# Performance work log

Measured on AMD Instinct MI355X. Metric: run time of the kernel, lower is better.

## Reference

```python
import jax, jax.numpy as jnp
import numpy as np

D_MODEL = 1024
D_STATE = 64
D_CONV = 4
HEADDIM = 64
EXPAND = 2
NGROUPS = 1
D_INNER = EXPAND * D_MODEL            # 2048
NHEADS = D_INNER // HEADDIM           # 32
CONV_DIM = D_INNER + 2 * NGROUPS * D_STATE
D_IN_PROJ = 2 * D_INNER + 2 * NGROUPS * D_STATE + NHEADS
FFN_DIM = 4096
B_SZ = 2
SEQ = 2048


def layernorm(x, w, b, eps=1e-5):
    m = jnp.mean(x, axis=-1, keepdims=True)
    v = jnp.var(x, axis=-1, keepdims=True)
    return (x - m) * jax.lax.rsqrt(v + eps) * w + b


def silu(x):
    return x * jax.nn.sigmoid(x)


def causal_dwconv(x, w, b):
    # x: [B, L, C], w: [C, K] depthwise, b: [C]; causal (left) padding
    xc = jnp.transpose(x, (0, 2, 1))                       # [B, C, L]
    xc = jnp.pad(xc, ((0, 0), (0, 0), (D_CONV - 1, 0)))
    k = w[:, None, :]                                      # [C, 1, K]
    y = jax.lax.conv_general_dilated(
        xc, k, window_strides=(1,), padding='VALID',
        dimension_numbers=('NCH', 'OIH', 'NCH'),
        feature_group_count=CONV_DIM)
    return jnp.transpose(y, (0, 2, 1)) + b                 # [B, L, C]


def mamba2(x, in_proj_w, conv_w, conv_b, dt_bias, A_log, D_param, norm_w, out_proj_w):
    Bsz, L, _ = x.shape
    zxbcdt = x @ in_proj_w.T                               # [B, L, D_IN_PROJ]
    z, xBC, dt = jnp.split(zxbcdt, [D_INNER, D_INNER + CONV_DIM], axis=-1)
    dt = jax.nn.softplus(dt + dt_bias)                     # [B, L, H]
    xBC = silu(causal_dwconv(xBC, conv_w, conv_b))
    xs, Bm, Cm = jnp.split(xBC, [D_INNER, D_INNER + NGROUPS * D_STATE], axis=-1)
    xs = xs.reshape(Bsz, L, NHEADS, HEADDIM)
    Bm = Bm.reshape(Bsz, L, NGROUPS, D_STATE)
    Cm = Cm.reshape(Bsz, L, NGROUPS, D_STATE)
    hpg = NHEADS // NGROUPS
    Bh = jnp.repeat(Bm, hpg, axis=2)                       # [B, L, H, N]
    Ch = jnp.repeat(Cm, hpg, axis=2)                       # [B, L, H, N]
    A = -jnp.exp(A_log)                                    # [H]
    dA = jnp.exp(dt * A)                                   # [B, L, H]

    # time-major for scan
    def step(h, inp):
        dA_t, dt_t, x_t, B_t, C_t = inp                    # [B,H], [B,H], [B,H,P], [B,H,N], [B,H,N]
        h = h * dA_t[:, :, None, None] + (dt_t[:, :, None, None] * x_t[..., None]) * B_t[:, :, None, :]
        y_t = jnp.einsum('bhpn,bhn->bhp', h, C_t)
        return h, y_t

    h0 = jnp.zeros((Bsz, NHEADS, HEADDIM, D_STATE), dtype=x.dtype)
    xs_tm = (jnp.moveaxis(dA, 1, 0), jnp.moveaxis(dt, 1, 0),
             jnp.moveaxis(xs, 1, 0), jnp.moveaxis(Bh, 1, 0), jnp.moveaxis(Ch, 1, 0))
    _, ys = jax.lax.scan(step, h0, xs_tm)                  # [L, B, H, P]
    y = jnp.moveaxis(ys, 0, 1) + D_param[None, None, :, None] * xs
    y = y.reshape(Bsz, L, D_INNER)
    # gated RMSNorm: RMSNorm(y * silu(z)) * weight
    y = y * silu(z)
    y = y * jax.lax.rsqrt(jnp.mean(jnp.square(y), axis=-1, keepdims=True) + 1e-5) * norm_w
    return y @ out_proj_w.T                                # [B, L, D_MODEL]


def setup_inputs() -> dict:
    key = jax.random.key(0)
    ks = jax.random.split(key, 12)
    s = 0.02
    inp = {
        'x': jax.random.normal(ks[0], (B_SZ, SEQ, D_MODEL), dtype=jnp.float32),
        'ln0_w': jnp.ones((D_MODEL,), jnp.float32), 'ln0_b': jnp.zeros((D_MODEL,), jnp.float32),
        'ln1_w': jnp.ones((D_MODEL,), jnp.float32), 'ln1_b': jnp.zeros((D_MODEL,), jnp.float32),
        'ln2_w': jnp.ones((D_MODEL,), jnp.float32), 'ln2_b': jnp.zeros((D_MODEL,), jnp.float32),
        'in_proj_w': jax.random.normal(ks[1], (D_IN_PROJ, D_MODEL), jnp.float32) * s,
        'conv_w': jax.random.normal(ks[2], (CONV_DIM, D_CONV), jnp.float32) * 0.2,
        'conv_b': jnp.zeros((CONV_DIM,), jnp.float32),
        'dt_bias': jax.random.uniform(ks[3], (NHEADS,), jnp.float32, -4.0, -1.0),
        'A_log': jnp.log(jnp.arange(1, NHEADS + 1, dtype=jnp.float32)),
        'D_param': jnp.ones((NHEADS,), jnp.float32),
        'norm_w': jnp.ones((D_INNER,), jnp.float32),
        'out_proj_w': jax.random.normal(ks[4], (D_MODEL, D_INNER), jnp.float32) * s,
        'ffn_w1': jax.random.normal(ks[5], (FFN_DIM, D_MODEL), jnp.float32) * s,
        'ffn_b1': jnp.zeros((FFN_DIM,), jnp.float32),
        'ffn_w2': jax.random.normal(ks[6], (D_MODEL, FFN_DIM), jnp.float32) * s,
        'ffn_b2': jnp.zeros((D_MODEL,), jnp.float32),
    }
    return inp


def reference(x, ln0_w, ln0_b, ln1_w, ln1_b, ln2_w, ln2_b, in_proj_w, conv_w, conv_b,
              dt_bias, A_log, D_param, norm_w, out_proj_w, ffn_w1, ffn_b1, ffn_w2, ffn_b2):
    x = layernorm(x, ln0_w, ln0_b)                                  # ln0 (layer_id==0)
    m = mamba2(layernorm(x, ln1_w, ln1_b), in_proj_w, conv_w, conv_b,
               dt_bias, A_log, D_param, norm_w, out_proj_w)
    x = x + m                                                        # dropout is identity in eval
    h = layernorm(x, ln2_w, ln2_b)
    h = jax.nn.gelu(h @ ffn_w1.T + ffn_b1, approximate=False) @ ffn_w2.T + ffn_b2
    return x + h
```

## Files before the change

### kernel.cpp

```cpp
#include <hip/hip_runtime.h>
#include <hip/hip_bf16.h>
#include <math.h>

typedef __hip_bfloat16 bf16;
typedef __bf16 bhalf;
typedef bhalf bhalf8 __attribute__((ext_vector_type(8)));
typedef float f32x4 __attribute__((ext_vector_type(4)));
typedef unsigned short u16;
typedef u16 u16x4 __attribute__((ext_vector_type(4)));

#define D_MODEL   1024
#define D_STATE   64
#define HEADDIM   64
#define D_INNER   2048
#define NHEADS    32
#define CONV_DIM  2176
#define D_IN_PROJ 4256
#define FFN_DIM   4096
#define BSZ       2
#define SEQ       2048
#define NROWS     (BSZ*SEQ)
#define TC        64
#define NCH       (SEQ/TC)

#define AS1 __attribute__((address_space(1)))
#define AS3 __attribute__((address_space(3)))
__device__ __forceinline__ void load_lds16(const void* g, void* l) {
  __builtin_amdgcn_global_load_lds((AS1 void*)g, (AS3 void*)l, 16, 0, 0);
}

__global__ __launch_bounds__(64)
void detect_kernel(const unsigned short* __restrict__ x, int* __restrict__ flagp)
{
  int bad = 0;
  for (int i = threadIdx.x; i < 4096; i += 64) {
    unsigned u = ((unsigned)x[i]) << 16;
    float v = __uint_as_float(u);
    if (!(fabsf(v) <= 1e6f)) bad = 1;
  }
  unsigned long long any = __ballot(bad);
  if (threadIdx.x == 0) *flagp = (any != 0ULL) ? 1 : 0;
}

#define NT 19
struct CvtArgs {
  const void* src[NT];
  void*       dst[NT];
  int ccum[NT + 1];
  int nel[NT];
};

__global__ __launch_bounds__(256)
void cvt_kernel(CvtArgs a, const int* __restrict__ flagp)
{
  int c = blockIdx.x;
  int ti = 0;
  while (c >= a.ccum[ti + 1]) ti++;
  int base = (c - a.ccum[ti]) * 2048;
  int n = a.nel[ti];
  if (*flagp) {
    const float* s = (const float*)a.src[ti];
    bf16* d = (bf16*)a.dst[ti];
    for (int i = threadIdx.x; i < 2048; i += 256) {
      int j = base + i;
      if (j < n) d[j] = __float2bfloat16(s[j]);
    }
  } else {
    const unsigned short* s = (const unsigned short*)a.src[ti];
    unsigned short* d = (unsigned short*)a.dst[ti];
    for (int i = threadIdx.x; i < 2048; i += 256) {
      int j = base + i;
      if (j < n) d[j] = s[j];
    }
  }
}

template<int EPI>
__global__ __launch_bounds__(256, 2)
void gemm_bt(const bf16* __restrict__ A, const bf16* __restrict__ W,
             int M, int N, int K, int nb,
             bf16* __restrict__ outB,
             const bf16* __restrict__ bias)
{
  __shared__ __align__(16) bhalf sA[128 * 64];
  __shared__ __align__(16) bhalf sW[128 * 64];
  const int id   = blockIdx.x;
  const int per  = nb * 8;
  const int hi   = id / per;
  const int rem  = id - hi * per;
  const int jn   = rem >> 3;
  const int mi   = hi * 8 + (rem & 7);
  const int n0   = jn * 128;
  const int m0   = mi * 128;
  const int t    = threadIdx.x;
  const int w    = t >> 6;
  const int lane = t & 63;
  const int wm   = (w >> 1) * 64;
  const int wn   = (w & 1) * 64;
  const int lr   = lane & 15;
  const int lq   = lane >> 4;

  f32x4 acc[4][4];
  #pragma unroll
  for (int i = 0; i < 4; i++)
    #pragma unroll
    for (int j = 0; j < 4; j++)
      acc[i][j] = (f32x4){0.f, 0.f, 0.f, 0.f};

  for (int k0 = 0; k0 < K; k0 += 64) {
    #pragma unroll
    for (int j = 0; j < 4; j++) {
      int s  = t + 256 * j;
      int r  = s >> 3;
      int cs = (s & 7) ^ (r & 7);
      load_lds16(A + (size_t)(m0 + r) * K + k0 + cs * 8, sA + s * 8);
      int wr = n0 + r; wr = wr < N ? wr : N - 1;
      load_lds16(W + (size_t)wr * K + k0 + cs * 8, sW + s * 8);
    }
    __syncthreads();
    #pragma unroll
    for (int kk = 0; kk < 2; kk++) {
      bhalf8 af[4], bfr[4];
      #pragma unroll
      for (int i = 0; i < 4; i++) {
        int r = wm + i * 16 + lr;
        int c = (kk * 4 + lq) ^ (r & 7);
        af[i] = *(const bhalf8*)(sA + r * 64 + c * 8);
      }
      #pragma unroll
      for (int j = 0; j < 4; j++) {
        int r = wn + j * 16 + lr;
        int c = (kk * 4 + lq) ^ (r & 7);
        bfr[j] = *(const bhalf8*)(sW + r * 64 + c * 8);
      }
      #pragma unroll
      for (int i = 0; i < 4; i++)
        #pragma unroll
        for (int j = 0; j < 4; j++)
          acc[i][j] = __builtin_amdgcn_mfma_f32_16x16x32_bf16(af[i], bfr[j], acc[i][j], 0, 0, 0);
    }
    __syncthreads();
  }

  #pragma unroll
  for (int i = 0; i < 4; i++) {
    #pragma unroll
    for (int j = 0; j < 4; j++) {
      #pragma unroll
      for (int r = 0; r < 4; r++) {
        int m = m0 + wm + i * 16 + lq * 4 + r;
        int n = n0 + wn + j * 16 + lr;
        if (n < N) {
          float v = acc[i][j][r];
          size_t idx = (size_t)m * N + n;
          if (EPI == 0) {
            outB[idx] = __float2bfloat16(v);
          } else {
            v += __bfloat162float(bias[n]);
            outB[idx] = __float2bfloat16(0.5f * v * (1.0f + erff(v * 0.70710678118654752f)));
          }
        }
      }
    }
  }
}

template<int EPI>
__global__ __launch_bounds__(256, 2)
void gemm_skinny(const bf16* __restrict__ A, const bf16* __restrict__ W,
                 int M, int N, int K,
                 float* __restrict__ outF, void* __restrict__ outAny,
                 const bf16* __restrict__ bias,
                 const bf16* __restrict__ resB,
                 const float* __restrict__ resF,
                 const int* __restrict__ flagp)
{
  __shared__ __align__(16) bhalf sA[64 * 64];
  __shared__ __align__(16) bhalf sW[128 * 64];
  const int id   = blockIdx.x;
  const int hi   = id >> 6;
  const int rem  = id & 63;
  const int jn   = rem >> 3;
  const int mi   = hi * 8 + (rem & 7);
  const int m0   = mi * 64;
  const int n0   = jn * 128;
  const int t    = threadIdx.x;
  const int w    = t >> 6;
  const int lane = t & 63;
  const int wm   = (w >> 1) * 32;
  const int wn   = (w & 1) * 64;
  const int lr   = lane & 15;
  const int lq   = lane >> 4;

  f32x4 acc[2][4];
  #pragma unroll
  for (int i = 0; i < 2; i++)
    #pragma unroll
    for (int j = 0; j < 4; j++)
      acc[i][j] = (f32x4){0.f, 0.f, 0.f, 0.f};

  for (int k0 = 0; k0 < K; k0 += 64) {
    {
      #pragma unroll
      for (int j = 0; j < 2; j++) {
        int s  = t + 256 * j;
        int r  = s >> 3;
        int cs = (s & 7) ^ (r & 7);
        load_lds16(A + (size_t)(m0 + r) * K + k0 + cs * 8, sA + s * 8);
      }
      #pragma unroll
      for (int j = 0; j < 4; j++) {
        int s  = t + 256 * j;
        int r  = s >> 3;
        int cs = (s & 7) ^ (r & 7);
        load_lds16(W + (size_t)(n0 + r) * K + k0 + cs * 8, sW + s * 8);
      }
    }
    __syncthreads();
    #pragma unroll
    for (int kk = 0; kk < 2; kk++) {
      bhalf8 af[2], bfr[4];
      #pragma unroll
      for (int i = 0; i < 2; i++) {
        int r = wm + i * 16 + lr;
        int c = (kk * 4 + lq) ^ (r & 7);
        af[i] = *(const bhalf8*)(sA + r * 64 + c * 8);
      }
      #pragma unroll
      for (int j = 0; j < 4; j++) {
        int r = wn + j * 16 + lr;
        int c = (kk * 4 + lq) ^ (r & 7);
        bfr[j] = *(const bhalf8*)(sW + r * 64 + c * 8);
      }
      #pragma unroll
      for (int i = 0; i < 2; i++)
        #pragma unroll
        for (int j = 0; j < 4; j++)
          acc[i][j] = __builtin_amdgcn_mfma_f32_16x16x32_bf16(af[i], bfr[j], acc[i][j], 0, 0, 0);
    }
    __syncthreads();
  }

  const bool f32o = (EPI == 1) && (*flagp != 0);
  #pragma unroll
  for (int i = 0; i < 2; i++) {
    #pragma unroll
    for (int j = 0; j < 4; j++) {
      #pragma unroll
      for (int r = 0; r < 4; r++) {
        int m = m0 + wm + i * 16 + lq * 4 + r;
        int n = n0 + wn + j * 16 + lr;
        size_t idx = (size_t)m * N + n;
        float v = acc[i][j][r];
        if (EPI == 0) {
          outF[idx] = v + __bfloat162float(resB[idx]);
        } else {
          v += __bfloat162float(bias[n]) + resF[idx];
          if (f32o) ((float*)outAny)[idx] = v;
          else      ((bf16*)outAny)[idx] = __float2bfloat16(v);
        }
      }
    }
  }
}

__global__ __launch_bounds__(256)
void ln01_kernel(const bf16* __restrict__ x,
                 const bf16* __restrict__ w0, const bf16* __restrict__ b0,
                 const bf16* __restrict__ w1, const bf16* __restrict__ b1,
                 bf16* __restrict__ x0o, bf16* __restrict__ x1o)
{
  int row = blockIdx.x, t = threadIdx.x;
  const bf16* xr = x + (size_t)row * D_MODEL;
  __shared__ float rs[4], rq[4];
  float v[4], s = 0.f, ss = 0.f;
  #pragma unroll
  for (int i = 0; i < 4; i++) {
    v[i] = __bfloat162float(xr[t + 256 * i]);
    s += v[i]; ss += v[i] * v[i];
  }
  #pragma unroll
  for (int o = 32; o; o >>= 1) { s += __shfl_down(s, o); ss += __shfl_down(ss, o); }
  if ((t & 63) == 0) { rs[t >> 6] = s; rq[t >> 6] = ss; }
  __syncthreads();
  float S = rs[0] + rs[1] + rs[2] + rs[3];
  float Q = rq[0] + rq[1] + rq[2] + rq[3];
  float mean = S * (1.f / D_MODEL);
  float rstd = rsqrtf(Q * (1.f / D_MODEL) - mean * mean + 1e-5f);
  float u[4]; s = 0.f; ss = 0.f;
  #pragma unroll
  for (int i = 0; i < 4; i++) {
    int c = t + 256 * i;
    u[i] = (v[i] - mean) * rstd * __bfloat162float(w0[c]) + __bfloat162float(b0[c]);
    s += u[i]; ss += u[i] * u[i];
    x0o[(size_t)row * D_MODEL + c] = __float2bfloat16(u[i]);
  }
  __syncthreads();
  #pragma unroll
  for (int o = 32; o; o >>= 1) { s += __shfl_down(s, o); ss += __shfl_down(ss, o); }
  if ((t & 63) == 0) { rs[t >> 6] = s; rq[t >> 6] = ss; }
  __syncthreads();
  S = rs[0] + rs[1] + rs[2] + rs[3];
  Q = rq[0] + rq[1] + rq[2] + rq[3];
  mean = S * (1.f / D_MODEL);
  rstd = rsqrtf(Q * (1.f / D_MODEL) - mean * mean + 1e-5f);
  #pragma unroll
  for (int i = 0; i < 4; i++) {
    int c = t + 256 * i;
    x1o[(size_t)row * D_MODEL + c] =
        __float2bfloat16((u[i] - mean) * rstd * __bfloat162float(w1[c]) + __bfloat162float(b1[c]));
  }
}

__global__ __launch_bounds__(256)
void conv_silu_kernel(const bf16* __restrict__ zxb, const bf16* __restrict__ cw,
                      const bf16* __restrict__ cb, bf16* __restrict__ xact)
{
  int c = blockIdx.x * 256 + threadIdx.x;
  int row = blockIdx.y;
  if (c >= CONV_DIM) return;
  int l = row & (SEQ - 1);
  float acc = __bfloat162float(cb[c]);
  #pragma unroll
  for (int k = 0; k < 4; k++) {
    int lt = l - 3 + k;
    if (lt >= 0)
      acc += __bfloat162float(zxb[(size_t)(row - 3 + k) * D_IN_PROJ + D_INNER + c]) *
             __bfloat162float(cw[c * 4 + k]);
  }
  xact[(size_t)row * CONV_DIM + c] = __float2bfloat16(acc / (1.f + expf(-acc)));
}

__global__ __launch_bounds__(256)
void dt_kernel(const bf16* __restrict__ zxb, const bf16* __restrict__ dt_bias,
               const bf16* __restrict__ A_log, float* __restrict__ dts,
               float* __restrict__ ldab)
{
  int i = blockIdx.x * 256 + threadIdx.x;
  int row = i >> 5, h = i & 31;
  float v = __bfloat162float(zxb[(size_t)row * D_IN_PROJ + (D_INNER + CONV_DIM) + h]) +
            __bfloat162float(dt_bias[h]);
  float sp = (v > 20.f) ? v : log1pf(expf(v));
  dts[i] = sp;
  ldab[i] = -sp * expf(__bfloat162float(A_log[h]));
}

__global__ __launch_bounds__(256)
void scan_state_kernel(const bf16* __restrict__ xact, const float* __restrict__ dts,
                       const float* __restrict__ ldab, bf16* __restrict__ Sbuf,
                       float* __restrict__ acb)
{
  __shared__ __align__(16) bf16 wBT[64][72];
  __shared__ __align__(16) bf16 XT[64][72];
  __shared__ float lsS[64], dtS[64];
  const int bid = blockIdx.x;
  const int bh = bid & 63, c = bid >> 6;
  const int b = bh >> 5, h = bh & 31;
  const int t0 = c * TC;
  const int tid = threadIdx.x;
  const int w = tid >> 6, lane = tid & 63;
  const int lr = lane & 15, lq = lane >> 4;

  if (w == 0) {
    float v = ldab[(size_t)(b * SEQ + t0 + lane) * NHEADS + h];
    #pragma unroll
    for (int o = 1; o < 64; o <<= 1) {
      float up = __shfl_up(v, o);
      if (lane >= o) v += up;
    }
    lsS[lane] = v;
    dtS[lane] = dts[(size_t)(b * SEQ + t0 + lane) * NHEADS + h];
  }
  __syncthreads();
  const float lsT = lsS[63];
  {
    int nn = tid & 63, u0 = (tid >> 6) * 16;
    for (int i = 0; i < 16; i++) {
      int u = u0 + i;
      const bf16* rowp = xact + (size_t)(b * SEQ + t0 + u) * CONV_DIM;
      float wgt = dtS[u] * __expf(lsT - lsS[u]);
      wBT[nn][u] = __float2bfloat16(__bfloat162float(rowp[D_INNER + nn]) * wgt);
      XT[nn][u]  = rowp[h * 64 + nn];
    }
  }
  __syncthreads();

  bhalf8 af0 = *(const bhalf8*)&wBT[16 * w + lr][lq * 8];
  bhalf8 af1 = *(const bhalf8*)&wBT[16 * w + lr][32 + lq * 8];
  bf16* sb = Sbuf + ((size_t)bh * NCH + c) * 4096;
  #pragma unroll
  for (int jt = 0; jt < 4; jt++) {
    bhalf8 xf0 = *(const bhalf8*)&XT[16 * jt + lr][lq * 8];
    bhalf8 xf1 = *(const bhalf8*)&XT[16 * jt + lr][32 + lq * 8];
    f32x4 acc = (f32x4){0.f, 0.f, 0.f, 0.f};
    acc = __builtin_amdgcn_mfma_f32_16x16x32_bf16(af0, xf0, acc, 0, 0, 0);
    acc = __builtin_amdgcn_mfma_f32_16x16x32_bf16(af1, xf1, acc, 0, 0, 0);
    #pragma unroll
    for (int r = 0; r < 4; r++) {
      int n = 16 * w + lq * 4 + r;
      int p = 16 * jt + lr;
      sb[p * 64 + n] = __float2bfloat16(acc[r]);
    }
  }
  if (tid == 0) acb[bh * NCH + c] = __expf(lsT);
}

__global__ __launch_bounds__(256)
void state_prop_kernel(bf16* __restrict__ Sbuf, const float* __restrict__ acb)
{
  const int bh = blockIdx.x >> 2, q = blockIdx.x & 3;
  const int t = threadIdx.x;
  bf16* sp = Sbuf + (size_t)bh * NCH * 4096 + q * 1024 + t;
  const float* ap = acb + bh * NCH;
  float h0 = 0.f, h1 = 0.f, h2 = 0.f, h3 = 0.f;
  for (int c = 0; c < NCH; c++) {
    bf16* pc = sp + (size_t)c * 4096;
    float s0 = __bfloat162float(pc[0]);
    float s1 = __bfloat162float(pc[256]);
    float s2 = __bfloat162float(pc[512]);
    float s3 = __bfloat162float(pc[768]);
    float a = ap[c];
    pc[0]   = __float2bfloat16(h0);
    pc[256] = __float2bfloat16(h1);
    pc[512] = __float2bfloat16(h2);
    pc[768] = __float2bfloat16(h3);
    h0 = fmaf(h0, a, s0); h1 = fmaf(h1, a, s1);
    h2 = fmaf(h2, a, s2); h3 = fmaf(h3, a, s3);
  }
}

__global__ __launch_bounds__(256)
void scan_y_kernel(const bf16* __restrict__ xact, const float* __restrict__ dts,
                   const float* __restrict__ ldab, const bf16* __restrict__ Sbuf,
                   bf16* __restrict__ yfull)
{
  __shared__ __align__(16) bf16 Cs[64][72];
  __shared__ __align__(16) bf16 Bs[64][72];
  __shared__ __align__(16) bf16 XT[64][72];
  __shared__ __align__(16) bf16 HT[64][72];
  __shared__ __align__(16) bf16 Ms[64][72];
  __shared__ float lsS[64], dtS[64];
  const int bid = blockIdx.x;
  const int bh = bid & 63, c = bid >> 6;
  const int b = bh >> 5, h = bh & 31;
  const int t0 = c * TC;
  const int tid = threadIdx.x;
  const int w = tid >> 6, lane = tid & 63;
  const int lr = lane & 15, lq = lane >> 4;

  if (w == 0) {
    float v = ldab[(size_t)(b * SEQ + t0 + lane) * NHEADS + h];
    #pragma unroll
    for (int o = 1; o < 64; o <<= 1) {
      float up = __shfl_up(v, o);
      if (lane >= o) v += up;
    }
    lsS[lane] = v;
    dtS[lane] = dts[(size_t)(b * SEQ + t0 + lane) * NHEADS + h];
  }
  {
    int nn = tid & 63, u0 = (tid >> 6) * 16;
    for (int i = 0; i < 16; i++) {
      int u = u0 + i;
      const bf16* rowp = xact + (size_t)(b * SEQ + t0 + u) * CONV_DIM;
      Bs[u][nn] = rowp[D_INNER + nn];
      Cs[u][nn] = rowp[D_INNER + 64 + nn];
      XT[nn][u] = rowp[h * 64 + nn];
    }
    const bf16* sb = Sbuf + ((size_t)bh * NCH + c) * 4096;
    for (int i = 0; i < 16; i++) {
      int e = tid + 256 * i;
      HT[e >> 6][e & 63] = sb[e];
    }
  }
  __syncthreads();

  bhalf8 cf0 = *(const bhalf8*)&Cs[16 * w + lr][lq * 8];
  bhalf8 cf1 = *(const bhalf8*)&Cs[16 * w + lr][32 + lq * 8];
  f32x4 accH[4];
  #pragma unroll
  for (int jt = 0; jt < 4; jt++) {
    bhalf8 bf0 = *(const bhalf8*)&Bs[16 * jt + lr][lq * 8];
    bhalf8 bf1 = *(const bhalf8*)&Bs[16 * jt + lr][32 + lq * 8];
    f32x4 g = (f32x4){0.f, 0.f, 0.f, 0.f};
    g = __builtin_amdgcn_mfma_f32_16x16x32_bf16(cf0, bf0, g, 0, 0, 0);
    g = __builtin_amdgcn_mfma_f32_16x16x32_bf16(cf1, bf1, g, 0, 0, 0);
    bhalf8 hf0 = *(const bhalf8*)&HT[16 * jt + lr][lq * 8];
    bhalf8 hf1 = *(const bhalf8*)&HT[16 * jt + lr][32 + lq * 8];
    f32x4 ah = (f32x4){0.f, 0.f, 0.f, 0.f};
    ah = __builtin_amdgcn_mfma_f32_16x16x32_bf16(cf0, hf0, ah, 0, 0, 0);
    ah = __builtin_amdgcn_mfma_f32_16x16x32_bf16(cf1, hf1, ah, 0, 0, 0);
    accH[jt] = ah;
    #pragma unroll
    for (int r = 0; r < 4; r++) {
      int t = 16 * w + lq * 4 + r;
      int u = 16 * jt + lr;
      float m = 0.f;
      if (u <= t) m = g[r] * __expf(lsS[t] - lsS[u]) * dtS[u];
      Ms[t][u] = __float2bfloat16(m);
    }
  }
  __syncthreads();

  bhalf8 mf0 = *(const bhalf8*)&Ms[16 * w + lr][lq * 8];
  bhalf8 mf1 = *(const bhalf8*)&Ms[16 * w + lr][32 + lq * 8];
  #pragma unroll
  for (int jt = 0; jt < 4; jt++) {
    bhalf8 xf0 = *(const bhalf8*)&XT[16 * jt + lr][lq * 8];
    bhalf8 xf1 = *(const bhalf8*)&XT[16 * jt + lr][32 + lq * 8];
    f32x4 acc = (f32x4){0.f, 0.f, 0.f, 0.f};
    acc = __builtin_amdgcn_mfma_f32_16x16x32_bf16(mf0, xf0, acc, 0, 0, 0);
    acc = __builtin_amdgcn_mfma_f32_16x16x32_bf16(mf1, xf1, acc, 0, 0, 0);
    #pragma unroll
    for (int r = 0; r < 4; r++) {
      int t = 16 * w + lq * 4 + r;
      int p = 16 * jt + lr;
      float y = acc[r] + __expf(lsS[t]) * accH[jt][r];
      yfull[(size_t)(b * SEQ + t0 + t) * D_INNER + h * 64 + p] = __float2bfloat16(y);
    }
  }
}

__global__ __launch_bounds__(256)
void gate_rms_kernel(const bf16* __restrict__ yfull, const bf16* __restrict__ xact,
                     const bf16* __restrict__ zxb, const bf16* __restrict__ Dp,
                     const bf16* __restrict__ nw, bf16* __restrict__ yn)
{
  int row = blockIdx.x, t = threadIdx.x;
  __shared__ float rq[4];
  float yv[8]; float ss = 0.f;
  #pragma unroll
  for (int i = 0; i < 8; i++) {
    int c = t + 256 * i;
    float y = __bfloat162float(yfull[(size_t)row * D_INNER + c]) +
              __bfloat162float(Dp[c >> 6]) *
              __bfloat162float(xact[(size_t)row * CONV_DIM + c]);
    float z = __bfloat162float(zxb[(size_t)row * D_IN_PROJ + c]);
    yv[i] = y * (z / (1.f + expf(-z)));
    ss += yv[i] * yv[i];
  }
  #pragma unroll
  for (int o = 32; o; o >>= 1) ss += __shfl_down(ss, o);
  if ((t & 63) == 0) rq[t >> 6] = ss;
  __syncthreads();
  float tot = rq[0] + rq[1] + rq[2] + rq[3];
  float rr = rsqrtf(tot * (1.f / D_INNER) + 1e-5f);
  #pragma unroll
  for (int i = 0; i < 8; i++) {
    int c = t + 256 * i;
    yn[(size_t)row * D_INNER + c] =
        __float2bfloat16(yv[i] * rr * __bfloat162float(nw[c]));
  }
}

__global__ __launch_bounds__(256)
void ln2_kernel(const float* __restrict__ xin, const bf16* __restrict__ w,
                const bf16* __restrict__ b, bf16* __restrict__ out)
{
  int row = blockIdx.x, t = threadIdx.x;
  const float* xr = xin + (size_t)row * D_MODEL;
  __shared__ float rs[4], rq[4];
  float v[4], s = 0.f, ss = 0.f;
  #pragma unroll
  for (int i = 0; i < 4; i++) {
    v[i] = xr[t + 256 * i];
    s += v[i]; ss += v[i] * v[i];
  }
  #pragma unroll
  for (int o = 32; o; o >>= 1) { s += __shfl_down(s, o); ss += __shfl_down(ss, o); }
  if ((t & 63) == 0) { rs[t >> 6] = s; rq[t >> 6] = ss; }
  __syncthreads();
  float S = rs[0] + rs[1] + rs[2] + rs[3];
  float Q = rq[0] + rq[1] + rq[2] + rq[3];
  float mean = S * (1.f / D_MODEL);
  float rstd = rsqrtf(Q * (1.f / D_MODEL) - mean * mean + 1e-5f);
  #pragma unroll
  for (int i = 0; i < 4; i++) {
    int c = t + 256 * i;
    out[(size_t)row * D_MODEL + c] =
        __float2bfloat16((v[i] - mean) * rstd * __bfloat162float(w[c]) + __bfloat162float(b[c]));
  }
}

extern "C" void kernel_launch(void* const* d_in, const int* in_sizes, int n_in,
                              void* d_out, int out_size, void* d_ws, size_t ws_size,
                              hipStream_t stream)
{
  char* ws = (char*)d_ws;
  bf16*  xcvt  = (bf16*) (ws + 0);
  bf16*  x1b   = (bf16*) (ws + 8388608);
  bf16*  Sbuf  = (bf16*) (ws + 0);
  bf16*  ynb   = (bf16*) (ws + 0);
  bf16*  wproj = (bf16*) (ws + 16777216);
  float* acb   = (float*)(ws + 16777216);
  float* dtsb  = (float*)(ws + 16785408);
  float* ldab  = (float*)(ws + 17309696);
  bf16*  wout  = (bf16*) (ws + 25493504);
  bf16*  w1c   = (bf16*) (ws + 29687808);
  bf16*  w2c   = (bf16*) (ws + 38076416);
  bf16*  ln0w  = (bf16*) (ws + 46465024);
  bf16*  ln0b  = (bf16*) (ws + 46467072);
  bf16*  ln1w  = (bf16*) (ws + 46469120);
  bf16*  ln1b  = (bf16*) (ws + 46471168);
  bf16*  ln2w  = (bf16*) (ws + 46473216);
  bf16*  ln2b  = (bf16*) (ws + 46475264);
  bf16*  convw = (bf16*) (ws + 46477312);
  bf16*  convb = (bf16*) (ws + 46494720);
  bf16*  dtb   = (bf16*) (ws + 46499072);
  bf16*  alog  = (bf16*) (ws + 46499136);
  bf16*  Dp    = (bf16*) (ws + 46499200);
  bf16*  normw = (bf16*) (ws + 46499264);
  bf16*  b1c   = (bf16*) (ws + 46503360);
  bf16*  b2c   = (bf16*) (ws + 46511552);
  int*   flag  = (int*)  (ws + 46513600);
  bf16*  x0b   = (bf16*) (ws + 46514176);
  bf16*  zxb   = (bf16*) (ws + 54902784);
  float* x2f   = (float*)(ws + 54902784);
  bf16*  xact  = (bf16*) (ws + 89767936);
  bf16*  gbuf  = (bf16*) (ws + 89767936);
  bf16*  yfull = (bf16*) (ws + 125419520);
  bf16*  hln   = (bf16*) (ws + 125419520);

  detect_kernel<<<1, 64, 0, stream>>>((const unsigned short*)d_in[0], flag);

  CvtArgs ca;
  void* dsts[NT] = { xcvt, ln0w, ln0b, ln1w, ln1b, ln2w, ln2b, wproj, convw, convb,
                     dtb, alog, Dp, normw, wout, w1c, b1c, w2c, b2c };
  int cc = 0;
  ca.ccum[0] = 0;
  for (int i = 0; i < NT; i++) {
    ca.src[i] = d_in[i];
    ca.dst[i] = dsts[i];
    ca.nel[i] = in_sizes[i];
    cc += (in_sizes[i] + 2047) / 2048;
    ca.ccum[i + 1] = cc;
  }
  cvt_kernel<<<cc, 256, 0, stream>>>(ca, flag);

  ln01_kernel<<<NROWS, 256, 0, stream>>>(xcvt, ln0w, ln0b, ln1w, ln1b, x0b, x1b);

  gemm_bt<0><<<34 * 32, 256, 0, stream>>>(x1b, wproj, NROWS, D_IN_PROJ, D_MODEL, 34,
                                          zxb, nullptr);

  conv_silu_kernel<<<dim3(9, NROWS), 256, 0, stream>>>(zxb, convw, convb, xact);
  dt_kernel<<<(NROWS * NHEADS) / 256, 256, 0, stream>>>(zxb, dtb, alog, dtsb, ldab);

  scan_state_kernel<<<NCH * 64, 256, 0, stream>>>(xact, dtsb, ldab, Sbuf, acb);
  state_prop_kernel<<<64 * 4, 256, 0, stream>>>(Sbuf, acb);
  scan_y_kernel<<<NCH * 64, 256, 0, stream>>>(xact, dtsb, ldab, Sbuf, yfull);

  gate_rms_kernel<<<NROWS, 256, 0, stream>>>(yfull, xact, zxb, Dp, normw, ynb);

  gemm_skinny<0><<<512, 256, 0, stream>>>(ynb, wout, NROWS, D_MODEL, D_INNER,
                                          x2f, nullptr, nullptr, x0b, nullptr, flag);

  ln2_kernel<<<NROWS, 256, 0, stream>>>(x2f, ln2w, ln2b, hln);

  gemm_bt<2><<<32 * 32, 256, 0, stream>>>(hln, w1c, NROWS, FFN_DIM, D_MODEL, 32,
                                          gbuf, b1c);

  gemm_skinny<1><<<512, 256, 0, stream>>>(gbuf, w2c, NROWS, D_MODEL, FFN_DIM,
                                          nullptr, d_out, b2c, nullptr, x2f, flag);
}
```

Measured before the change: 477.8 us.

## Split-K skinny GEMMs with fused reduce+LN2, fuse conv/dt, skip x conversion

The two N=1024 GEMMs now split K in half and launch 1024 blocks, with occupancy hint 4, to fill more CUs. Each half writes fp32 partials, and separate reduce kernels add them together with the residual and bias. The out-proj reduce also performs LayerNorm2. The dt computation is folded into the conv+SiLU kernel, and ln01 reads the raw input directly instead of a converted copy. The split adds fp32 partial traffic and extra launches in exchange for better GEMM parallelism.

```diff
diff --git a/kernel.cpp b/kernel.cpp
--- a/kernel.cpp
+++ b/kernel.cpp
@@ -42,7 +42,7 @@
   if (threadIdx.x == 0) *flagp = (any != 0ULL) ? 1 : 0;
 }
 
-#define NT 19
+#define NT 18
 struct CvtArgs {
   const void* src[NT];
   void*       dst[NT];
@@ -165,21 +165,18 @@
   }
 }
 
-template<int EPI>
-__global__ __launch_bounds__(256, 2)
-void gemm_skinny(const bf16* __restrict__ A, const bf16* __restrict__ W,
-                 int M, int N, int K,
-                 float* __restrict__ outF, void* __restrict__ outAny,
-                 const bf16* __restrict__ bias,
-                 const bf16* __restrict__ resB,
-                 const float* __restrict__ resF,
-                 const int* __restrict__ flagp)
+__global__ __launch_bounds__(256, 4)
+void gemm_skinny_sk(const bf16* __restrict__ A, const bf16* __restrict__ W,
+                    int M, int N, int K,
+                    float* __restrict__ p0, float* __restrict__ p1)
 {
   __shared__ __align__(16) bhalf sA[64 * 64];
   __shared__ __align__(16) bhalf sW[128 * 64];
   const int id   = blockIdx.x;
-  const int hi   = id >> 6;
-  const int rem  = id & 63;
+  const int z    = id >> 9;
+  const int id9  = id & 511;
+  const int hi   = id9 >> 6;
+  const int rem  = id9 & 63;
   const int jn   = rem >> 3;
   const int mi   = hi * 8 + (rem & 7);
   const int m0   = mi * 64;
@@ -199,22 +196,22 @@
     for (int j = 0; j < 4; j++)
       acc[i][j] = (f32x4){0.f, 0.f, 0.f, 0.f};
 
-  for (int k0 = 0; k0 < K; k0 += 64) {
-    {
-      #pragma unroll
-      for (int j = 0; j < 2; j++) {
-        int s  = t + 256 * j;
-        int r  = s >> 3;
-        int cs = (s & 7) ^ (r & 7);
-        load_lds16(A + (size_t)(m0 + r) * K + k0 + cs * 8, sA + s * 8);
-      }
-      #pragma unroll
-      for (int j = 0; j < 4; j++) {
-        int s  = t + 256 * j;
-        int r  = s >> 3;
-        int cs = (s & 7) ^ (r & 7);
-        load_lds16(W + (size_t)(n0 + r) * K + k0 + cs * 8, sW + s * 8);
-      }
+  const int kh = K >> 1;
+  const int kend = z * kh + kh;
+  for (int k0 = z * kh; k0 < kend; k0 += 64) {
+    #pragma unroll
+    for (int j = 0; j < 2; j++) {
+      int s  = t + 256 * j;
+      int r  = s >> 3;
+      int cs = (s & 7) ^ (r & 7);
+      load_lds16(A + (size_t)(m0 + r) * K + k0 + cs * 8, sA + s * 8);
+    }
+    #pragma unroll
+    for (int j = 0; j < 4; j++) {
+      int s  = t + 256 * j;
+      int r  = s >> 3;
+      int cs = (s & 7) ^ (r & 7);
+      load_lds16(W + (size_t)(n0 + r) * K + k0 + cs * 8, sW + s * 8);
     }
     __syncthreads();
     #pragma unroll
@@ -241,44 +238,102 @@
     __syncthreads();
   }
 
-  const bool f32o = (EPI == 1) && (*flagp != 0);
-  #pragma unroll
-  for (int i = 0; i < 2; i++) {
-    #pragma unroll
-    for (int j = 0; j < 4; j++) {
+  float* out = z ? p1 : p0;
+  #pragma unroll
+  for (int i = 0; i < 2; i++)
+    #pragma unroll
+    for (int j = 0; j < 4; j++)
       #pragma unroll
       for (int r = 0; r < 4; r++) {
         int m = m0 + wm + i * 16 + lq * 4 + r;
         int n = n0 + wn + j * 16 + lr;
-        size_t idx = (size_t)m * N + n;
-        float v = acc[i][j][r];
-        if (EPI == 0) {
-          outF[idx] = v + __bfloat162float(resB[idx]);
-        } else {
-          v += __bfloat162float(bias[n]) + resF[idx];
-          if (f32o) ((float*)outAny)[idx] = v;
-          else      ((bf16*)outAny)[idx] = __float2bfloat16(v);
-        }
+        out[(size_t)m * N + n] = acc[i][j][r];
       }
-    }
-  }
-}
-
-__global__ __launch_bounds__(256)
-void ln01_kernel(const bf16* __restrict__ x,
+}
+
+__global__ __launch_bounds__(256)
+void reduce_out_ln2_kernel(const float* __restrict__ p0, const float* __restrict__ p1,
+                           const bf16* __restrict__ resB, float* __restrict__ x2f,
+                           const bf16* __restrict__ w, const bf16* __restrict__ b,
+                           bf16* __restrict__ hln)
+{
+  int row = blockIdx.x, t = threadIdx.x;
+  int i = row * 256 + t;
+  __shared__ float rs[4], rq[4];
+  f32x4 a = ((const f32x4*)p0)[i];
+  f32x4 bb = ((const f32x4*)p1)[i];
+  u16x4 r = ((const u16x4*)resB)[i];
+  f32x4 o;
+  float s = 0.f, ss = 0.f;
+  #pragma unroll
+  for (int j = 0; j < 4; j++) {
+    o[j] = a[j] + bb[j] + __uint_as_float(((unsigned)r[j]) << 16);
+    s += o[j]; ss += o[j] * o[j];
+  }
+  ((f32x4*)x2f)[i] = o;
+  #pragma unroll
+  for (int off = 32; off; off >>= 1) { s += __shfl_down(s, off); ss += __shfl_down(ss, off); }
+  if ((t & 63) == 0) { rs[t >> 6] = s; rq[t >> 6] = ss; }
+  __syncthreads();
+  float S = rs[0] + rs[1] + rs[2] + rs[3];
+  float Q = rq[0] + rq[1] + rq[2] + rq[3];
+  float mean = S * (1.f / D_MODEL);
+  float rstd = rsqrtf(Q * (1.f / D_MODEL) - mean * mean + 1e-5f);
+  u16x4 wv = ((const u16x4*)w)[t];
+  u16x4 bv = ((const u16x4*)b)[t];
+  #pragma unroll
+  for (int j = 0; j < 4; j++) {
+    float wj = __uint_as_float(((unsigned)wv[j]) << 16);
+    float bj = __uint_as_float(((unsigned)bv[j]) << 16);
+    hln[(size_t)row * D_MODEL + t * 4 + j] =
+        __float2bfloat16((o[j] - mean) * rstd * wj + bj);
+  }
+}
+
+__global__ __launch_bounds__(256)
+void reduce_ffn_kernel(const float* __restrict__ p0, const float* __restrict__ p1,
+                       const bf16* __restrict__ bias, const float* __restrict__ resF,
+                       void* __restrict__ outp, const int* __restrict__ flagp)
+{
+  int i = blockIdx.x * 256 + threadIdx.x;
+  int n4 = i & (D_MODEL / 4 - 1);
+  f32x4 v0 = ((const f32x4*)p0)[i];
+  f32x4 v1 = ((const f32x4*)p1)[i];
+  f32x4 rf = ((const f32x4*)resF)[i];
+  u16x4 bb = ((const u16x4*)bias)[n4];
+  f32x4 o;
+  #pragma unroll
+  for (int j = 0; j < 4; j++)
+    o[j] = v0[j] + v1[j] + rf[j] + __uint_as_float(((unsigned)bb[j]) << 16);
+  if (*flagp) {
+    ((f32x4*)outp)[i] = o;
+  } else {
+    bf16* ob = (bf16*)outp;
+    #pragma unroll
+    for (int j = 0; j < 4; j++) ob[i * 4 + j] = __float2bfloat16(o[j]);
+  }
+}
+
+__global__ __launch_bounds__(256)
+void ln01_kernel(const void* __restrict__ xin, const int* __restrict__ flagp,
                  const bf16* __restrict__ w0, const bf16* __restrict__ b0,
                  const bf16* __restrict__ w1, const bf16* __restrict__ b1,
                  bf16* __restrict__ x0o, bf16* __restrict__ x1o)
 {
   int row = blockIdx.x, t = threadIdx.x;
-  const bf16* xr = x + (size_t)row * D_MODEL;
   __shared__ float rs[4], rq[4];
   float v[4], s = 0.f, ss = 0.f;
-  #pragma unroll
-  for (int i = 0; i < 4; i++) {
-    v[i] = __bfloat162float(xr[t + 256 * i]);
-    s += v[i]; ss += v[i] * v[i];
-  }
+  if (*flagp) {
+    const float* xr = (const float*)xin + (size_t)row * D_MODEL;
+    #pragma unroll
+    for (int i = 0; i < 4; i++) v[i] = xr[t + 256 * i];
+  } else {
+    const bf16* xr = (const bf16*)xin + (size_t)row * D_MODEL;
+    #pragma unroll
+    for (int i = 0; i < 4; i++) v[i] = __bfloat162float(xr[t + 256 * i]);
+  }
+  #pragma unroll
+  for (int i = 0; i < 4; i++) { s += v[i]; ss += v[i] * v[i]; }
   #pragma unroll
   for (int o = 32; o; o >>= 1) { s += __shfl_down(s, o); ss += __shfl_down(ss, o); }
   if ((t & 63) == 0) { rs[t >> 6] = s; rq[t >> 6] = ss; }
@@ -313,36 +368,32 @@
 }
 
 __global__ __launch_bounds__(256)
-void conv_silu_kernel(const bf16* __restrict__ zxb, const bf16* __restrict__ cw,
-                      const bf16* __restrict__ cb, bf16* __restrict__ xact)
+void conv_silu_dt_kernel(const bf16* __restrict__ zxb, const bf16* __restrict__ cw,
+                         const bf16* __restrict__ cb, bf16* __restrict__ xact,
+                         const bf16* __restrict__ dtb, const bf16* __restrict__ alog,
+                         float* __restrict__ dts, float* __restrict__ ldab)
 {
   int c = blockIdx.x * 256 + threadIdx.x;
   int row = blockIdx.y;
-  if (c >= CONV_DIM) return;
-  int l = row & (SEQ - 1);
-  float acc = __bfloat162float(cb[c]);
-  #pragma unroll
-  for (int k = 0; k < 4; k++) {
-    int lt = l - 3 + k;
-    if (lt >= 0)
-      acc += __bfloat162float(zxb[(size_t)(row - 3 + k) * D_IN_PROJ + D_INNER + c]) *
-             __bfloat162float(cw[c * 4 + k]);
-  }
-  xact[(size_t)row * CONV_DIM + c] = __float2bfloat16(acc / (1.f + expf(-acc)));
-}
-
-__global__ __launch_bounds__(256)
-void dt_kernel(const bf16* __restrict__ zxb, const bf16* __restrict__ dt_bias,
-               const bf16* __restrict__ A_log, float* __restrict__ dts,
-               float* __restrict__ ldab)
-{
-  int i = blockIdx.x * 256 + threadIdx.x;
-  int row = i >> 5, h = i & 31;
-  float v = __bfloat162float(zxb[(size_t)row * D_IN_PROJ + (D_INNER + CONV_DIM) + h]) +
-            __bfloat162float(dt_bias[h]);
-  float sp = (v > 20.f) ? v : log1pf(expf(v));
-  dts[i] = sp;
-  ldab[i] = -sp * expf(__bfloat162float(A_log[h]));
+  if (c < CONV_DIM) {
+    int l = row & (SEQ - 1);
+    float acc = __bfloat162float(cb[c]);
+    #pragma unroll
+    for (int k = 0; k < 4; k++) {
+      int lt = l - 3 + k;
+      if (lt >= 0)
+        acc += __bfloat162float(zxb[(size_t)(row - 3 + k) * D_IN_PROJ + D_INNER + c]) *
+               __bfloat162float(cw[c * 4 + k]);
+    }
+    xact[(size_t)row * CONV_DIM + c] = __float2bfloat16(acc / (1.f + expf(-acc)));
+  } else if (c < CONV_DIM + NHEADS) {
+    int h = c - CONV_DIM;
+    float v = __bfloat162float(zxb[(size_t)row * D_IN_PROJ + (D_INNER + CONV_DIM) + h]) +
+              __bfloat162float(dtb[h]);
+    float sp = (v > 20.f) ? v : log1pf(expf(v));
+    dts[row * NHEADS + h] = sp;
+    ldab[row * NHEADS + h] = -sp * expf(__bfloat162float(alog[h]));
+  }
 }
 
 __global__ __launch_bounds__(256)
@@ -553,48 +604,20 @@
   }
 }
 
-__global__ __launch_bounds__(256)
-void ln2_kernel(const float* __restrict__ xin, const bf16* __restrict__ w,
-                const bf16* __restrict__ b, bf16* __restrict__ out)
-{
-  int row = blockIdx.x, t = threadIdx.x;
-  const float* xr = xin + (size_t)row * D_MODEL;
-  __shared__ float rs[4], rq[4];
-  float v[4], s = 0.f, ss = 0.f;
-  #pragma unroll
-  for (int i = 0; i < 4; i++) {
-    v[i] = xr[t + 256 * i];
-    s += v[i]; ss += v[i] * v[i];
-  }
-  #pragma unroll
-  for (int o = 32; o; o >>= 1) { s += __shfl_down(s, o); ss += __shfl_down(ss, o); }
-  if ((t & 63) == 0) { rs[t >> 6] = s; rq[t >> 6] = ss; }
-  __syncthreads();
-  float S = rs[0] + rs[1] + rs[2] + rs[3];
-  float Q = rq[0] + rq[1] + rq[2] + rq[3];
-  float mean = S * (1.f / D_MODEL);
-  float rstd = rsqrtf(Q * (1.f / D_MODEL) - mean * mean + 1e-5f);
-  #pragma unroll
-  for (int i = 0; i < 4; i++) {
-    int c = t + 256 * i;
-    out[(size_t)row * D_MODEL + c] =
-        __float2bfloat16((v[i] - mean) * rstd * __bfloat162float(w[c]) + __bfloat162float(b[c]));
-  }
-}
-
 extern "C" void kernel_launch(void* const* d_in, const int* in_sizes, int n_in,
                               void* d_out, int out_size, void* d_ws, size_t ws_size,
                               hipStream_t stream)
 {
   char* ws = (char*)d_ws;
-  bf16*  xcvt  = (bf16*) (ws + 0);
-  bf16*  x1b   = (bf16*) (ws + 8388608);
+  bf16*  x1b   = (bf16*) (ws + 0);
   bf16*  Sbuf  = (bf16*) (ws + 0);
   bf16*  ynb   = (bf16*) (ws + 0);
+  float* pf0   = (float*)(ws + 0);
   bf16*  wproj = (bf16*) (ws + 16777216);
   float* acb   = (float*)(ws + 16777216);
   float* dtsb  = (float*)(ws + 16785408);
   float* ldab  = (float*)(ws + 17309696);
+  float* pf1   = (float*)(ws + 16777216);
   bf16*  wout  = (bf16*) (ws + 25493504);
   bf16*  w1c   = (bf16*) (ws + 29687808);
   bf16*  w2c   = (bf16*) (ws + 38076416);
@@ -617,6 +640,8 @@
   bf16*  zxb   = (bf16*) (ws + 54902784);
   float* x2f   = (float*)(ws + 54902784);
   bf16*  xact  = (bf16*) (ws + 89767936);
+  float* pout0 = (float*)(ws + 89767936);
+  float* pout1 = (float*)(ws + 106545152);
   bf16*  gbuf  = (bf16*) (ws + 89767936);
   bf16*  yfull = (bf16*) (ws + 125419520);
   bf16*  hln   = (bf16*) (ws + 125419520);
@@ -624,26 +649,27 @@
   detect_kernel<<<1, 64, 0, stream>>>((const unsigned short*)d_in[0], flag);
 
   CvtArgs ca;
-  void* dsts[NT] = { xcvt, ln0w, ln0b, ln1w, ln1b, ln2w, ln2b, wproj, convw, convb,
+  void* dsts[NT] = { ln0w, ln0b, ln1w, ln1b, ln2w, ln2b, wproj, convw, convb,
                      dtb, alog, Dp, normw, wout, w1c, b1c, w2c, b2c };
   int cc = 0;
   ca.ccum[0] = 0;
   for (int i = 0; i < NT; i++) {
-    ca.src[i] = d_in[i];
+    ca.src[i] = d_in[i + 1];
     ca.dst[i] = dsts[i];
-    ca.nel[i] = in_sizes[i];
-    cc += (in_sizes[i] + 2047) / 2048;
+    ca.nel[i] = in_sizes[i + 1];
+    cc += (in_sizes[i + 1] + 2047) / 2048;
     ca.ccum[i + 1] = cc;
   }
   cvt_kernel<<<cc, 256, 0, stream>>>(ca, flag);
 
-  ln01_kernel<<<NROWS, 256, 0, stream>>>(xcvt, ln0w, ln0b, ln1w, ln1b, x0b, x1b);
+  ln01_kernel<<<NROWS, 256, 0, stream>>>(d_in[0], flag, ln0w, ln0b, ln1w, ln1b,
+                                         x0b, x1b);
 
   gemm_bt<0><<<34 * 32, 256, 0, stream>>>(x1b, wproj, NROWS, D_IN_PROJ, D_MODEL, 34,
                                           zxb, nullptr);
 
-  conv_silu_kernel<<<dim3(9, NROWS), 256, 0, stream>>>(zxb, convw, convb, xact);
-  dt_kernel<<<(NROWS * NHEADS) / 256, 256, 0, stream>>>(zxb, dtb, alog, dtsb, ldab);
+  conv_silu_dt_kernel<<<dim3(9, NROWS), 256, 0, stream>>>(zxb, convw, convb, xact,
+                                                          dtb, alog, dtsb, ldab);
 
   scan_state_kernel<<<NCH * 64, 256, 0, stream>>>(xact, dtsb, ldab, Sbuf, acb);
   state_prop_kernel<<<64 * 4, 256, 0, stream>>>(Sbuf, acb);
@@ -651,14 +677,16 @@
 
   gate_rms_kernel<<<NROWS, 256, 0, stream>>>(yfull, xact, zxb, Dp, normw, ynb);
 
-  gemm_skinny<0><<<512, 256, 0, stream>>>(ynb, wout, NROWS, D_MODEL, D_INNER,
-                                          x2f, nullptr, nullptr, x0b, nullptr, flag);
-
-  ln2_kernel<<<NROWS, 256, 0, stream>>>(x2f, ln2w, ln2b, hln);
+  gemm_skinny_sk<<<1024, 256, 0, stream>>>(ynb, wout, NROWS, D_MODEL, D_INNER,
+                                           pout0, pout1);
+  reduce_out_ln2_kernel<<<NROWS, 256, 0, stream>>>(pout0, pout1, x0b, x2f,
+                                                   ln2w, ln2b, hln);
 
   gemm_bt<2><<<32 * 32, 256, 0, stream>>>(hln, w1c, NROWS, FFN_DIM, D_MODEL, 32,
                                           gbuf, b1c);
 
-  gemm_skinny<1><<<512, 256, 0, stream>>>(gbuf, w2c, NROWS, D_MODEL, FFN_DIM,
-                                          nullptr, d_out, b2c, nullptr, x2f, flag);
-}
+  gemm_skinny_sk<<<1024, 256, 0, stream>>>(gbuf, w2c, NROWS, D_MODEL, FFN_DIM,
+                                           pf0, pf1);
+  reduce_ffn_kernel<<<(NROWS * D_MODEL) / 1024, 256, 0, stream>>>(pf0, pf1,
+                                                                  b2c, x2f, d_out, flag);
+}
```

Result: faster. 455.6 us (-4.7%).
